# Performance work log

Measured on AMD Instinct MI355X. Metric: run time of the kernel, lower is better.

Reference implementation:

```python
import jax, jax.numpy as jnp
import numpy as np

B, N, K, NB = 8, 4096, 16, 8
MAX_RADIUS = 10.0
OUT_MUL = 64  # irreps_out = '64x1o' -> output dim 64*3 = 192


def setup_inputs() -> dict:
    key = jax.random.key(0)
    k1, k2 = jax.random.split(key)
    coords = jax.random.normal(k1, (B, N, 3), dtype=jnp.float32)
    tp_weight = jax.random.normal(k2, (1, NB, OUT_MUL), dtype=jnp.float32)
    return {"coords": coords, "tp_weight": tp_weight}


def _knn_indices(coords, k):
    # coords: [B, N, 3] -> nbr idx [B, N, k] (no self loops), per-batch kNN
    n = coords.shape[1]
    d2 = jnp.sum((coords[:, :, None, :] - coords[:, None, :, :]) ** 2, axis=-1)  # [B,N,N]
    d2 = jnp.where(jnp.eye(n, dtype=bool)[None], jnp.inf, d2)
    _, idx = jax.lax.top_k(-d2, k)  # k nearest
    return idx


def reference(coords, tp_weight):
    nbr = _knn_indices(coords, K)                                # [B,N,K] int32
    nbr_coords = jax.vmap(lambda c, i: c[i])(coords, nbr)        # [B,N,K,3]
    r = nbr_coords - coords[:, :, None, :]                       # sender - receiver
    dist = jnp.linalg.norm(r, axis=-1, keepdims=True)            # [B,N,K,1]
    rhat = r / (dist + 1e-8)                                     # 1x1o input
    cutoff = jnp.clip(dist / MAX_RADIUS, 0.0, 1.0)
    # gaussian soft one-hot over [0,1] with NB centers
    centers = jnp.linspace(0.0, 1.0, NB, dtype=coords.dtype)
    sigma = 1.0 / NB
    g = jnp.exp(-((cutoff - centers) ** 2) / (2.0 * sigma * sigma))  # [B,N,K,NB]
    s = jnp.sum(g, axis=-1, keepdims=True)
    rb = g / jnp.where(s > 0, s, jnp.ones_like(s))               # 8x0e input
    # FullyConnectedTensorProduct 1x1o x NBx0e -> OUT_MULx1o (shared weights)
    # path normalization: 1/sqrt(mul_in1 * mul_in2) = 1/sqrt(NB)
    alpha = 1.0 / np.sqrt(1 * NB)
    W = tp_weight[0]                                             # [NB, OUT_MUL]
    edge_feat = alpha * jnp.einsum('vw,bnkv,bnkm->bnkwm', W, rb, rhat)  # [B,N,K,64,3]
    # exactly k incoming edges per receiver -> scatter_mean == mean over K
    agg = jnp.mean(edge_feat, axis=2).reshape(B, N, OUT_MUL * 3)  # [B,N,192]
    return agg
```

## Files before the change

kernel.cpp:

```cpp
#include <hip/hip_runtime.h>

typedef unsigned int u32;
typedef unsigned long long u64;
typedef float v2f __attribute__((ext_vector_type(2)));

#define NBATCH 8
#define NPTS   4096
#define NQTOT  (NBATCH * NPTS)
#define KNN    16
#define NBASIS 8
#define OUTM   64
#define NSPLIT 8
#define WIN    (NPTS / NSPLIT)
#define QPB    64
#define TKNN   (QPB * NSPLIT)
#define GRP    8
#define ECAP   64
#define ROWSTR 81
#define TOFF   64

#define SENT 0x7f800000ffffffffull

__device__ __forceinline__ void ce(u64& x, u64& y) {
  u64 a = x, b = y;
  bool sw = b < a;
  x = sw ? b : a;
  y = sw ? a : b;
}

template <int N>
__device__ __forceinline__ void oems_sort(u64* a) {
#pragma unroll
  for (int p = 1; p < N; p <<= 1) {
#pragma unroll
    for (int k = p; k >= 1; k >>= 1) {
#pragma unroll
      for (int j = k & (p - 1); j + k < N; j += 2 * k) {
#pragma unroll
        for (int i = 0; i < k; ++i) {
          int lo = i + j, hi = i + j + k;
          if (hi < N && (lo / (2 * p)) == (hi / (2 * p)))
            ce(a[lo], a[hi]);
        }
      }
    }
  }
}

__device__ __forceinline__ void merge16(u64 t[16], const u64 a[16]) {
  u64 m[16];
#pragma unroll
  for (int i = 0; i < 16; ++i) {
    u64 x = t[i], y = a[15 - i];
    m[i] = (x < y) ? x : y;
  }
#pragma unroll
  for (int k = 8; k >= 1; k >>= 1) {
#pragma unroll
    for (int i = 0; i < 16; ++i) {
      if ((i & k) == 0) ce(m[i], m[i | k]);
    }
  }
#pragma unroll
  for (int i = 0; i < 16; ++i) t[i] = m[i];
}

__device__ __forceinline__ v2f d2pair(v2f cx, v2f cy, v2f cz, v2f qx, v2f qy,
                                      v2f qz) {
#pragma clang fp contract(off)
  v2f dx = cx - qx;
  v2f dy = cy - qy;
  v2f dz = cz - qz;
  v2f d2 = (dx * dx + dy * dy) + dz * dz;
  return d2;
}

__device__ __forceinline__ float d2s(float cx, float cy, float cz, float qx,
                                     float qy, float qz) {
#pragma clang fp contract(off)
  float dx = cx - qx;
  float dy = cy - qy;
  float dz = cz - qz;
  return (dx * dx + dy * dy) + dz * dz;
}

__global__ __launch_bounds__(TKNN) void se3_kernel(
    const float* __restrict__ Xp, const float* __restrict__ Yp,
    const float* __restrict__ Zp, const float4* __restrict__ cpad,
    const float* __restrict__ Wmat, float* __restrict__ out) {
  __shared__ u64 sBuf[QPB * ROWSTR];
  __shared__ u32 sCnt[QPB];
  __shared__ float sThr[QPB];
  __shared__ float sM[QPB * 25];

  const int b = blockIdx.x;
  const int qg = blockIdx.y;
  const int tid = threadIdx.x;
  const int ql = tid & 63;
  const int sp = tid >> 6;
  const int qi = qg * QPB + ql;
  const int base = b * NPTS;

  if (tid < QPB) sCnt[tid] = 0;

  const float qx = Xp[base + qi];
  const float qy = Yp[base + qi];
  const float qz = Zp[base + qi];
  const v2f qxx = {qx, qx}, qyy = {qy, qy}, qzz = {qz, qz};

  const int wbase = __builtin_amdgcn_readfirstlane(sp * WIN);
  const v2f* xs2 = (const v2f*)(Xp + base + wbase);
  const v2f* ys2 = (const v2f*)(Yp + base + wbase);
  const v2f* zs2 = (const v2f*)(Zp + base + wbase);
  const int sj = qi - wbase;

  u64* row = sBuf + (size_t)ql * ROWSTR;

  {
    u64 s16[16];
    float cd[16];
#pragma unroll
    for (int p = 0; p < 8; ++p) {
      v2f d2 = d2pair(xs2[p], ys2[p], zs2[p], qxx, qyy, qzz);
      cd[2 * p + 0] = d2.x;
      cd[2 * p + 1] = d2.y;
    }
#pragma unroll
    for (int i = 0; i < 16; ++i) {
      u64 v = ((u64)__float_as_uint(cd[i]) << 32) | (u32)(wbase + i);
      s16[i] = (i == sj) ? SENT : v;
    }
    oems_sort<16>(s16);

    if (sp >= 1 && sp <= 4) {
#pragma unroll
      for (int e = 0; e < 16; ++e) row[(sp - 1) * 16 + e] = s16[e];
    }
    __syncthreads();
    if (sp == 0) {
      u64 t16[16];
#pragma unroll
      for (int e = 0; e < 16; ++e) t16[e] = s16[e];
#pragma unroll
      for (int s = 0; s < 4; ++s) {
        u64 a[16];
#pragma unroll
        for (int e = 0; e < 16; ++e) a[e] = row[s * 16 + e];
        merge16(t16, a);
      }
#pragma unroll
      for (int e = 0; e < 16; ++e) row[TOFF + e] = t16[e];
    }
    __syncthreads();
    if (sp >= 5) {
#pragma unroll
      for (int e = 0; e < 16; ++e) row[(sp - 5) * 16 + e] = s16[e];
    }
    __syncthreads();
    if (sp == 0) {
      u64 t16[16];
#pragma unroll
      for (int e = 0; e < 16; ++e) t16[e] = row[TOFF + e];
#pragma unroll
      for (int s = 0; s < 3; ++s) {
        u64 a[16];
#pragma unroll
        for (int e = 0; e < 16; ++e) a[e] = row[s * 16 + e];
        merge16(t16, a);
      }
#pragma unroll
      for (int e = 0; e < 16; ++e) row[TOFF + e] = t16[e];
      sThr[ql] = __uint_as_float((u32)(t16[15] >> 32));
    }
    __syncthreads();
  }
  float thr = sThr[ql];

  const int selfgrp = (sj >= 0 && sj < WIN) ? (sj >> 3) : -1;
  const u32 selfbit = 1u << (sj & 7);

  u32* ebuf = (u32*)row;

#pragma unroll
  for (int ph = 0; ph < 5; ++ph) {
    const int cstart = 16 << ph;
    const int cend = 32 << ph;
#pragma unroll 2
    for (int g = cstart; g < cend; g += GRP) {
      v2f d2p[4];
#pragma unroll
      for (int p = 0; p < 4; ++p)
        d2p[p] = d2pair(xs2[(g >> 1) + p], ys2[(g >> 1) + p],
                        zs2[(g >> 1) + p], qxx, qyy, qzz);
      u32 want = 0;
#pragma unroll
      for (int i = 0; i < GRP; ++i)
        want |= (d2p[i >> 1][i & 1] <= thr) ? (1u << i) : 0u;
      if ((g >> 3) == selfgrp) want &= ~selfbit;
      if (want) {
        u32 slot = atomicAdd(&sCnt[ql], 1u);
        if (slot < ECAP) ebuf[slot] = (want << 12) | (u32)(wbase + g);
      }
    }
    __syncthreads();
    if (sp == ph + 1) {
      int n = (int)sCnt[ql];
      n = n < ECAP ? n : ECAP;
      if (__any(n > 0)) {
        u64 t16[16];
#pragma unroll
        for (int e = 0; e < 16; ++e) t16[e] = row[TOFF + e];
        int cursor = 0;
        u32 curWant = 0, curBase = 0;
        while (__any(cursor < n || curWant != 0)) {
          u32 kidx[16];
          u32 vmask = 0;
#pragma unroll
          for (int e = 0; e < 16; ++e) {
            if (curWant == 0 && cursor < n) {
              u32 ent = ebuf[cursor++];
              curWant = ent >> 12;
              curBase = ent & 0xFFFu;
            }
            if (curWant) {
              int bit = __ffs(curWant) - 1;
              curWant &= curWant - 1;
              kidx[e] = curBase + (u32)bit;
              vmask |= (1u << e);
            } else {
              kidx[e] = 0;
            }
          }
          u64 a[16];
#pragma unroll
          for (int e = 0; e < 16; ++e) {
            float4 c = cpad[base + (int)kidx[e]];
            float d2 = d2s(c.x, c.y, c.z, qx, qy, qz);
            u64 key = ((u64)__float_as_uint(d2) << 32) | kidx[e];
            a[e] = (vmask & (1u << e)) ? key : SENT;
          }
          oems_sort<16>(a);
          merge16(t16, a);
        }
#pragma unroll
        for (int e = 0; e < 16; ++e) row[TOFF + e] = t16[e];
        sThr[ql] = __uint_as_float((u32)(t16[15] >> 32));
      }
      sCnt[ql] = 0;
    }
    __syncthreads();
    thr = sThr[ql];
  }

  if (sp < 4) {
    const int k = sp;
    u64 pv[4];
#pragma unroll
    for (int e = 0; e < 4; ++e) pv[e] = row[TOFF + k * 4 + e];
    float4 nc[4];
    float dd[4];
#pragma unroll
    for (int e = 0; e < 4; ++e) {
      nc[e] = cpad[base + (int)(u32)pv[e]];
      dd[e] = __uint_as_float((u32)(pv[e] >> 32));
    }
    float M[24];
#pragma unroll
    for (int j = 0; j < 24; ++j) M[j] = 0.f;
#pragma unroll
    for (int e = 0; e < 4; ++e) {
      float rx = nc[e].x - qx;
      float ry = nc[e].y - qy;
      float rz = nc[e].z - qz;
      float dist = sqrtf(dd[e]);
      float inv = 1.0f / (dist + 1e-8f);
      rx *= inv; ry *= inv; rz *= inv;
      float cut = fminf(dist * 0.1f, 1.0f);
      float g[NBASIS], s = 0.f;
#pragma unroll
      for (int v = 0; v < NBASIS; ++v) {
        float t = cut - (float)v * (1.0f / 7.0f);
        g[v] = __expf(-32.0f * t * t);
        s += g[v];
      }
      float rs = 1.0f / s;
#pragma unroll
      for (int v = 0; v < NBASIS; ++v) {
        float rb = g[v] * rs;
        M[v * 3 + 0] = fmaf(rb, rx, M[v * 3 + 0]);
        M[v * 3 + 1] = fmaf(rb, ry, M[v * 3 + 1]);
        M[v * 3 + 2] = fmaf(rb, rz, M[v * 3 + 2]);
      }
    }
    float* fp = (float*)row;
#pragma unroll
    for (int c = 0; c < 24; ++c) fp[k * 25 + c] = M[c];
  }
  __syncthreads();

  {
    const float* fp = (const float*)row;
#pragma unroll
    for (int j0 = 0; j0 < 3; ++j0) {
      int j = sp * 3 + j0;
      float s = fp[0 * 25 + j] + fp[1 * 25 + j] + fp[2 * 25 + j] +
                fp[3 * 25 + j];
      sM[ql * 25 + j] = s;
    }
  }
  __syncthreads();

  float wreg[NBASIS];
#pragma unroll
  for (int v = 0; v < NBASIS; ++v) wreg[v] = Wmat[v * OUTM + ql];
  const float scale = 0.022097086912079608f;
#pragma unroll
  for (int i = 0; i < 8; ++i) {
    int q = sp * 8 + i;
    const float* mq = sM + q * 25;
    float a0 = 0.f, a1 = 0.f, a2 = 0.f;
#pragma unroll
    for (int v = 0; v < NBASIS; ++v) {
      a0 = fmaf(wreg[v], mq[v * 3 + 0], a0);
      a1 = fmaf(wreg[v], mq[v * 3 + 1], a1);
      a2 = fmaf(wreg[v], mq[v * 3 + 2], a2);
    }
    size_t o = (size_t)(base + qg * QPB + q) * (OUTM * 3) + ql * 3;
    out[o + 0] = a0 * scale;
    out[o + 1] = a1 * scale;
    out[o + 2] = a2 * scale;
  }
}

__global__ void prep_kernel(const float* __restrict__ coords,
                            float* __restrict__ Xp, float* __restrict__ Yp,
                            float* __restrict__ Zp, float4* __restrict__ cpad) {
  int i = blockIdx.x * 256 + threadIdx.x;
  if (i < NQTOT) {
    float x = coords[3 * i + 0];
    float y = coords[3 * i + 1];
    float z = coords[3 * i + 2];
    Xp[i] = x; Yp[i] = y; Zp[i] = z;
    cpad[i] = make_float4(x, y, z, 0.f);
  }
}

extern "C" void kernel_launch(void* const* d_in, const int* in_sizes, int n_in,
                              void* d_out, int out_size, void* d_ws, size_t ws_size,
                              hipStream_t stream) {
  const float* coords = (const float*)d_in[0];
  const float* Wmat = (const float*)d_in[1];
  float* out = (float*)d_out;

  char* w = (char*)d_ws;
  float* Xp = (float*)(w);
  float* Yp = (float*)(w + 131072);
  float* Zp = (float*)(w + 262144);
  float4* cpad = (float4*)(w + 393216);

  prep_kernel<<<dim3((NQTOT + 255) / 256), dim3(256), 0, stream>>>(coords, Xp, Yp, Zp, cpad);
  se3_kernel<<<dim3(NBATCH, NPTS / QPB), dim3(TKNN), 0, stream>>>(Xp, Yp, Zp, cpad, Wmat, out);
}
```

Baseline: 170.6 us.

## Add dedicated merge wavefront and double-buffer candidate lists to overlap scan and merge

Adds a ninth wavefront per block that merges candidate lists while the eight scanning wavefronts move on to the next distance phase. Candidate buffers and counters are double-buffered by phase parity, and scanners re-read the threshold through a volatile pointer on every group. Before, the merge ran serially on one scanning wavefront between barriers. Scanners now filter against a threshold that lags by one phase, so they may emit more candidates; the capacity is raised to 96 and the shared-memory row grows.

```diff
diff --git a/kernel.cpp b/kernel.cpp
--- a/kernel.cpp
+++ b/kernel.cpp
@@ -13,11 +13,11 @@
 #define NSPLIT 8
 #define WIN    (NPTS / NSPLIT)
 #define QPB    64
-#define TKNN   (QPB * NSPLIT)
+#define TKNN   (QPB * NSPLIT + 64)
 #define GRP    8
-#define ECAP   64
-#define ROWSTR 81
-#define TOFF   64
+#define ECAP   96
+#define ROWSTR 113
+#define TOFF   96
 
 #define SENT 0x7f800000ffffffffull
 
@@ -89,7 +89,7 @@
     const float* __restrict__ Zp, const float4* __restrict__ cpad,
     const float* __restrict__ Wmat, float* __restrict__ out) {
   __shared__ u64 sBuf[QPB * ROWSTR];
-  __shared__ u32 sCnt[QPB];
+  __shared__ u32 sCnt[2 * QPB];
   __shared__ float sThr[QPB];
   __shared__ float sM[QPB * 25];
 
@@ -101,14 +101,14 @@
   const int qi = qg * QPB + ql;
   const int base = b * NPTS;
 
-  if (tid < QPB) sCnt[tid] = 0;
+  if (tid < 2 * QPB) sCnt[tid] = 0;
 
   const float qx = Xp[base + qi];
   const float qy = Yp[base + qi];
   const float qz = Zp[base + qi];
   const v2f qxx = {qx, qx}, qyy = {qy, qy}, qzz = {qz, qz};
 
-  const int wbase = __builtin_amdgcn_readfirstlane(sp * WIN);
+  const int wbase = __builtin_amdgcn_readfirstlane((sp & 7) * WIN);
   const v2f* xs2 = (const v2f*)(Xp + base + wbase);
   const v2f* ys2 = (const v2f*)(Yp + base + wbase);
   const v2f* zs2 = (const v2f*)(Zp + base + wbase);
@@ -118,19 +118,21 @@
 
   {
     u64 s16[16];
-    float cd[16];
-#pragma unroll
-    for (int p = 0; p < 8; ++p) {
-      v2f d2 = d2pair(xs2[p], ys2[p], zs2[p], qxx, qyy, qzz);
-      cd[2 * p + 0] = d2.x;
-      cd[2 * p + 1] = d2.y;
-    }
-#pragma unroll
-    for (int i = 0; i < 16; ++i) {
-      u64 v = ((u64)__float_as_uint(cd[i]) << 32) | (u32)(wbase + i);
-      s16[i] = (i == sj) ? SENT : v;
-    }
-    oems_sort<16>(s16);
+    if (sp < 8) {
+      float cd[16];
+#pragma unroll
+      for (int p = 0; p < 8; ++p) {
+        v2f d2 = d2pair(xs2[p], ys2[p], zs2[p], qxx, qyy, qzz);
+        cd[2 * p + 0] = d2.x;
+        cd[2 * p + 1] = d2.y;
+      }
+#pragma unroll
+      for (int i = 0; i < 16; ++i) {
+        u64 v = ((u64)__float_as_uint(cd[i]) << 32) | (u32)(wbase + i);
+        s16[i] = (i == sj) ? SENT : v;
+      }
+      oems_sort<16>(s16);
+    }
 
     if (sp >= 1 && sp <= 4) {
 #pragma unroll
@@ -152,7 +154,7 @@
       for (int e = 0; e < 16; ++e) row[TOFF + e] = t16[e];
     }
     __syncthreads();
-    if (sp >= 5) {
+    if (sp >= 5 && sp < 8) {
 #pragma unroll
       for (int e = 0; e < 16; ++e) row[(sp - 5) * 16 + e] = s16[e];
     }
@@ -174,82 +176,84 @@
     }
     __syncthreads();
   }
-  float thr = sThr[ql];
 
   const int selfgrp = (sj >= 0 && sj < WIN) ? (sj >> 3) : -1;
   const u32 selfbit = 1u << (sj & 7);
 
-  u32* ebuf = (u32*)row;
-
-#pragma unroll
-  for (int ph = 0; ph < 5; ++ph) {
-    const int cstart = 16 << ph;
-    const int cend = 32 << ph;
+  volatile float* vThr = sThr;
+
+#pragma unroll
+  for (int ph = 0; ph <= 5; ++ph) {
+    if (sp < 8 && ph < 5) {
+      const int cb = ph & 1;
+      u32* ebuf = (u32*)row + cb * ECAP;
+      u32* cnt = &sCnt[cb * QPB + ql];
+      const int cstart = 16 << ph;
+      const int cend = 32 << ph;
 #pragma unroll 2
-    for (int g = cstart; g < cend; g += GRP) {
-      v2f d2p[4];
-#pragma unroll
-      for (int p = 0; p < 4; ++p)
-        d2p[p] = d2pair(xs2[(g >> 1) + p], ys2[(g >> 1) + p],
-                        zs2[(g >> 1) + p], qxx, qyy, qzz);
-      u32 want = 0;
-#pragma unroll
-      for (int i = 0; i < GRP; ++i)
-        want |= (d2p[i >> 1][i & 1] <= thr) ? (1u << i) : 0u;
-      if ((g >> 3) == selfgrp) want &= ~selfbit;
-      if (want) {
-        u32 slot = atomicAdd(&sCnt[ql], 1u);
-        if (slot < ECAP) ebuf[slot] = (want << 12) | (u32)(wbase + g);
-      }
-    }
-    __syncthreads();
-    if (sp == ph + 1) {
-      int n = (int)sCnt[ql];
+      for (int g = cstart; g < cend; g += GRP) {
+        v2f d2p[4];
+#pragma unroll
+        for (int p = 0; p < 4; ++p)
+          d2p[p] = d2pair(xs2[(g >> 1) + p], ys2[(g >> 1) + p],
+                          zs2[(g >> 1) + p], qxx, qyy, qzz);
+        float thr = vThr[ql];
+        u32 want = 0;
+#pragma unroll
+        for (int i = 0; i < GRP; ++i)
+          want |= (d2p[i >> 1][i & 1] <= thr) ? (1u << i) : 0u;
+        if ((g >> 3) == selfgrp) want &= ~selfbit;
+        if (want) {
+          u32 slot = atomicAdd(cnt, 1u);
+          if (slot < ECAP) ebuf[slot] = (want << 12) | (u32)(wbase + g);
+        }
+      }
+    } else if (sp == 8 && ph >= 1) {
+      const int pb = (ph - 1) & 1;
+      const u32* ebuf = (const u32*)row + pb * ECAP;
+      int n = (int)sCnt[pb * QPB + ql];
       n = n < ECAP ? n : ECAP;
-      if (__any(n > 0)) {
-        u64 t16[16];
-#pragma unroll
-        for (int e = 0; e < 16; ++e) t16[e] = row[TOFF + e];
-        int cursor = 0;
-        u32 curWant = 0, curBase = 0;
-        while (__any(cursor < n || curWant != 0)) {
-          u32 kidx[16];
-          u32 vmask = 0;
-#pragma unroll
-          for (int e = 0; e < 16; ++e) {
-            if (curWant == 0 && cursor < n) {
-              u32 ent = ebuf[cursor++];
-              curWant = ent >> 12;
-              curBase = ent & 0xFFFu;
-            }
-            if (curWant) {
-              int bit = __ffs(curWant) - 1;
-              curWant &= curWant - 1;
-              kidx[e] = curBase + (u32)bit;
-              vmask |= (1u << e);
-            } else {
-              kidx[e] = 0;
-            }
+      u64 t16[16];
+#pragma unroll
+      for (int e = 0; e < 16; ++e) t16[e] = row[TOFF + e];
+      int cursor = 0;
+      u32 curWant = 0, curBase = 0;
+      while (__any(cursor < n || curWant != 0)) {
+        u32 kidx[16];
+        u32 vmask = 0;
+#pragma unroll
+        for (int e = 0; e < 16; ++e) {
+          if (curWant == 0 && cursor < n) {
+            u32 ent = ebuf[cursor++];
+            curWant = ent >> 12;
+            curBase = ent & 0xFFFu;
           }
-          u64 a[16];
-#pragma unroll
-          for (int e = 0; e < 16; ++e) {
-            float4 c = cpad[base + (int)kidx[e]];
-            float d2 = d2s(c.x, c.y, c.z, qx, qy, qz);
-            u64 key = ((u64)__float_as_uint(d2) << 32) | kidx[e];
-            a[e] = (vmask & (1u << e)) ? key : SENT;
+          if (curWant) {
+            int bit = __ffs(curWant) - 1;
+            curWant &= curWant - 1;
+            kidx[e] = curBase + (u32)bit;
+            vmask |= (1u << e);
+          } else {
+            kidx[e] = 0;
           }
-          oems_sort<16>(a);
-          merge16(t16, a);
         }
-#pragma unroll
-        for (int e = 0; e < 16; ++e) row[TOFF + e] = t16[e];
-        sThr[ql] = __uint_as_float((u32)(t16[15] >> 32));
-      }
-      sCnt[ql] = 0;
-    }
-    __syncthreads();
-    thr = sThr[ql];
+        u64 a[16];
+#pragma unroll
+        for (int e = 0; e < 16; ++e) {
+          float4 c = cpad[base + (int)kidx[e]];
+          float d2 = d2s(c.x, c.y, c.z, qx, qy, qz);
+          u64 key = ((u64)__float_as_uint(d2) << 32) | kidx[e];
+          a[e] = (vmask & (1u << e)) ? key : SENT;
+        }
+        oems_sort<16>(a);
+        merge16(t16, a);
+      }
+#pragma unroll
+      for (int e = 0; e < 16; ++e) row[TOFF + e] = t16[e];
+      sThr[ql] = __uint_as_float((u32)(t16[15] >> 32));
+      sCnt[pb * QPB + ql] = 0;
+    }
+    __syncthreads();
   }
 
   if (sp < 4) {
@@ -298,7 +302,7 @@
   }
   __syncthreads();
 
-  {
+  if (sp < 8) {
     const float* fp = (const float*)row;
 #pragma unroll
     for (int j0 = 0; j0 < 3; ++j0) {
@@ -310,25 +314,27 @@
   }
   __syncthreads();
 
-  float wreg[NBASIS];
-#pragma unroll
-  for (int v = 0; v < NBASIS; ++v) wreg[v] = Wmat[v * OUTM + ql];
-  const float scale = 0.022097086912079608f;
-#pragma unroll
-  for (int i = 0; i < 8; ++i) {
-    int q = sp * 8 + i;
-    const float* mq = sM + q * 25;
-    float a0 = 0.f, a1 = 0.f, a2 = 0.f;
-#pragma unroll
-    for (int v = 0; v < NBASIS; ++v) {
-      a0 = fmaf(wreg[v], mq[v * 3 + 0], a0);
-      a1 = fmaf(wreg[v], mq[v * 3 + 1], a1);
-      a2 = fmaf(wreg[v], mq[v * 3 + 2], a2);
-    }
-    size_t o = (size_t)(base + qg * QPB + q) * (OUTM * 3) + ql * 3;
-    out[o + 0] = a0 * scale;
-    out[o + 1] = a1 * scale;
-    out[o + 2] = a2 * scale;
+  if (sp < 8) {
+    float wreg[NBASIS];
+#pragma unroll
+    for (int v = 0; v < NBASIS; ++v) wreg[v] = Wmat[v * OUTM + ql];
+    const float scale = 0.022097086912079608f;
+#pragma unroll
+    for (int i = 0; i < 8; ++i) {
+      int q = sp * 8 + i;
+      const float* mq = sM + q * 25;
+      float a0 = 0.f, a1 = 0.f, a2 = 0.f;
+#pragma unroll
+      for (int v = 0; v < NBASIS; ++v) {
+        a0 = fmaf(wreg[v], mq[v * 3 + 0], a0);
+        a1 = fmaf(wreg[v], mq[v * 3 + 1], a1);
+        a2 = fmaf(wreg[v], mq[v * 3 + 2], a2);
+      }
+      size_t o = (size_t)(base + qg * QPB + q) * (OUTM * 3) + ql * 3;
+      out[o + 0] = a0 * scale;
+      out[o + 1] = a1 * scale;
+      out[o + 2] = a2 * scale;
+    }
   }
 }
 
```

Measured after the change: 253.0 us. 48.3% more time.
